# Kernel optimization log

Hardware: AMD Instinct MI355X
Metric: run time of the kernel (lower is better)

The kernel has to match this reference:

```python
import jax, jax.numpy as jnp
import numpy as np

N_NODES = 4096
N_EDGES = 16384
L = 512
MP_STEPS = 5
DT = 0.01


def _mlp(x, W1, b1, W2, b2):
    return jax.nn.relu(x @ W1 + b1) @ W2 + b2


def _ln(x):
    m = jnp.mean(x, axis=-1, keepdims=True)
    v = jnp.var(x, axis=-1, keepdims=True)
    return (x - m) * jax.lax.rsqrt(v + 1e-6)


_PARAM_SHAPES = [
    ("enc_e_W1", (1, L)), ("enc_e_b1", (L,)), ("enc_e_W2", (L, L)), ("enc_e_b2", (L,)),
    ("enc_n_W1", (1, L)), ("enc_n_b1", (L,)), ("enc_n_W2", (L, L)), ("enc_n_b2", (L,)),
    ("proc_e_W1", (3 * L, L)), ("proc_e_b1", (L,)), ("proc_e_W2", (L, L)), ("proc_e_b2", (L,)),
    ("proc_n_W1", (2 * L, L)), ("proc_n_b1", (L,)), ("proc_n_W2", (L, L)), ("proc_n_b2", (L,)),
    ("dec_e_W1", (L, L)), ("dec_e_b1", (L,)), ("dec_e_W2", (L, 1)), ("dec_e_b2", (1,)),
]


def setup_inputs() -> dict:
    key = jax.random.key(0)
    ks = jax.random.split(key, 3 + len(_PARAM_SHAPES))
    d = {}
    d["state"] = jax.random.normal(ks[0], (N_EDGES + N_NODES,), dtype=jnp.float32)
    d["senders"] = jax.random.randint(ks[1], (N_EDGES,), 0, N_NODES)
    d["receivers"] = jax.random.randint(ks[2], (N_EDGES,), 0, N_NODES)
    for i, (name, shp) in enumerate(_PARAM_SHAPES):
        if name.endswith(("b1", "b2")):
            d[name] = jnp.zeros(shp, dtype=jnp.float32)
        else:
            d[name] = 0.02 * jax.random.normal(ks[3 + i], shp, dtype=jnp.float32)
    return d


def _hamiltonian(x, senders, receivers,
                 enc_e_W1, enc_e_b1, enc_e_W2, enc_e_b2,
                 enc_n_W1, enc_n_b1, enc_n_W2, enc_n_b2,
                 proc_e_W1, proc_e_b1, proc_e_W2, proc_e_b2,
                 proc_n_W1, proc_n_b1, proc_n_W2, proc_n_b2,
                 dec_e_W1, dec_e_b1, dec_e_W2, dec_e_b2):
    # graph_from_state: edge scalars then node scalars
    e = x[:N_EDGES].reshape(N_EDGES, 1)
    n = x[N_EDGES:].reshape(N_NODES, 1)
    # encode (MLP + layer norm)
    eh = _ln(_mlp(e, enc_e_W1, enc_e_b1, enc_e_W2, enc_e_b2))  # [E, L]
    nh = _ln(_mlp(n, enc_n_W1, enc_n_b1, enc_n_W2, enc_n_b2))  # [N, L]
    # process: num_mp_steps of GraphNetwork-style message passing, shared params
    for _ in range(MP_STEPS):
        msg_in = jnp.concatenate([eh, nh[senders], nh[receivers]], axis=-1)  # [E, 3L]
        eh = eh + _mlp(msg_in, proc_e_W1, proc_e_b1, proc_e_W2, proc_e_b2)
        agg = jax.ops.segment_sum(eh, receivers, num_segments=N_NODES)  # [N, L]
        node_in = jnp.concatenate([nh, agg], axis=-1)  # [N, 2L]
        nh = nh + _mlp(node_in, proc_n_W1, proc_n_b1, proc_n_W2, proc_n_b2)
    # decode edges to scalars; H = sum of decoded edge energies
    dec_e = _mlp(eh, dec_e_W1, dec_e_b1, dec_e_W2, dec_e_b2)  # [E, 1]
    return jnp.sum(dec_e)


def reference(state, senders, receivers,
              enc_e_W1, enc_e_b1, enc_e_W2, enc_e_b2,
              enc_n_W1, enc_n_b1, enc_n_W2, enc_n_b2,
              proc_e_W1, proc_e_b1, proc_e_W2, proc_e_b2,
              proc_n_W1, proc_n_b1, proc_n_W2, proc_n_b2,
              dec_e_W1, dec_e_b1, dec_e_W2, dec_e_b2):
    def H_fn(x):
        return _hamiltonian(x, senders, receivers,
                            enc_e_W1, enc_e_b1, enc_e_W2, enc_e_b2,
                            enc_n_W1, enc_n_b1, enc_n_W2, enc_n_b2,
                            proc_e_W1, proc_e_b1, proc_e_W2, proc_e_b2,
                            proc_n_W1, proc_n_b1, proc_n_W2, proc_n_b2,
                            dec_e_W1, dec_e_b1, dec_e_W2, dec_e_b2)
    H, dH = jax.value_and_grad(H_fn)(state)
    # one integrator step driven by the Hamiltonian gradient (stand-in for DAE solve)
    next_state = state - DT * dH
    return next_state
```

## Files before the change

### kernel.cpp

```cpp
#include <hip/hip_runtime.h>


#define E_ROWS 16384
#define N_ROWS 4096
#define ALL_ROWS 20480
#define DT_F   0.01f

typedef unsigned char u8;
typedef unsigned short u16;
typedef unsigned long long u64;
typedef __attribute__((ext_vector_type(8))) short short8v;
typedef __attribute__((ext_vector_type(4))) float f32x4;

__device__ __forceinline__ u16 f2b(float f) {
    union { float f; unsigned u; } v; v.f = f;
    unsigned r = v.u + 0x7FFF + ((v.u >> 16) & 1);
    return (u16)(r >> 16);
}
__device__ __forceinline__ float b2f(u16 u) {
    union { unsigned u; float f; } v; v.u = ((unsigned)u) << 16;
    return v.f;
}
__device__ __forceinline__ void gld16(const u16* g, u16* l) {
    __builtin_amdgcn_global_load_lds((const __attribute__((address_space(1))) void*)g,
                                     (__attribute__((address_space(3))) void*)l, 16, 0, 0);
}
template<int N> __device__ __forceinline__ void waitcnt_vm() {
    if constexpr (N == 0)      asm volatile("s_waitcnt vmcnt(0)" ::: "memory");
    else if constexpr (N == 2) asm volatile("s_waitcnt vmcnt(2)" ::: "memory");
    else if constexpr (N == 4) asm volatile("s_waitcnt vmcnt(4)" ::: "memory");
    else if constexpr (N == 8) asm volatile("s_waitcnt vmcnt(8)" ::: "memory");
}

template<int BM, int WM, int WN, int KTOT, int LDA, int LDC,
         bool ADD_C, bool GATHER2, bool BIAS, bool RELU_MASK, bool APPLY_MASK,
         bool WF32, bool WBF16, bool DUALOUT, bool ROWDOT, bool DECW2, bool BSEL>
__global__ __launch_bounds__(256)
void bgemm(const u16* __restrict__ A, const u16* __restrict__ Bt, const u16* __restrict__ Bt2,
           float* __restrict__ C, u16* __restrict__ Cb,
           const u16* __restrict__ Cinb, const float* __restrict__ bias,
           const float* __restrict__ bias2, const u16* __restrict__ G12b,
           const int* __restrict__ sidx, const int* __restrict__ ridx,
           u8* __restrict__ maskw, u16* __restrict__ C2b,
           const float* __restrict__ wvec, const float* __restrict__ wvec2,
           float* __restrict__ outp)
{
    constexpr int BN = WN * 64;
    constexpr int NA = BM / 16;
    constexpr int TC = (BM + BN) / 16;
    constexpr int PER = TC / 4;
    constexpr int NT = KTOT / 32;
    constexpr int IFRAG = BM / WM / 16;
    constexpr int BUFU = TC * 512;
    constexpr int LSZ = (3 * BUFU > BM * BN) ? 3 * BUFU : BM * BN;
    __shared__ u16 Ls[LSZ];

    const int tid = threadIdx.x;
    const int lane = tid & 63;
    const int wv = tid >> 6;
    const int wr = wv / WN;
    const int wc = wv % WN;

    const int gx = gridDim.x;
    int id = blockIdx.y * gx + blockIdx.x;
    const int nwg = gx * gridDim.y;
    id = (id & 7) * (nwg >> 3) + (id >> 3);
    const int bx = id % gx;
    const int by = id / gx;
    const int rowBase = by * BM;
    const int colBase = bx * BN;

    const u16* BtU = Bt;
    const float* biasU = bias;
    const float* wvecU = wvec;
    if (BSEL && rowBase >= E_ROWS) { BtU = Bt2; biasU = bias2; wvecU = wvec2; }

    const int srow = lane & 15;
    const int slotk = (lane >> 4) << 3;

    const u16* srcs[PER];
    int dstoff[PER];
#pragma unroll
    for (int q = 0; q < PER; ++q) {
        const int c = wv + (q << 2);
        if (c < NA)
            srcs[q] = A + (size_t)(rowBase + c * 16 + srow) * LDA + slotk;
        else
            srcs[q] = BtU + (size_t)(colBase + (c - NA) * 16 + srow) * KTOT + slotk;
        dstoff[q] = c * 512;
    }

    f32x4 acc[IFRAG][4];
#pragma unroll
    for (int i = 0; i < IFRAG; ++i)
#pragma unroll
        for (int j = 0; j < 4; ++j)
            acc[i][j] = (f32x4){0.f, 0.f, 0.f, 0.f};

    const int fro = ((lane >> 4) << 7) + ((lane & 15) << 3);

#pragma unroll
    for (int q = 0; q < PER; ++q) gld16(srcs[q], &Ls[dstoff[q]]);
#pragma unroll
    for (int q = 0; q < PER; ++q) gld16(srcs[q] + 32, &Ls[BUFU + dstoff[q]]);
    waitcnt_vm<PER>();
    __builtin_amdgcn_s_barrier();
    asm volatile("" ::: "memory");

    for (int t = 0; t < NT; ++t) {
        const int cur = t % 3;
        if (t + 2 < NT) {
            const int nxt = (t + 2) % 3;
#pragma unroll
            for (int q = 0; q < PER; ++q)
                gld16(srcs[q] + (t + 2) * 32, &Ls[nxt * BUFU + dstoff[q]]);
        }
        const u16* Lc = &Ls[cur * BUFU];
        short8v af[IFRAG], bfm[4];
#pragma unroll
        for (int i = 0; i < IFRAG; ++i)
            af[i] = *(const short8v*)&Lc[((wr * IFRAG + i) << 9) + fro];
#pragma unroll
        for (int j = 0; j < 4; ++j)
            bfm[j] = *(const short8v*)&Lc[((NA + (wc << 2) + j) << 9) + fro];
#pragma unroll
        for (int i = 0; i < IFRAG; ++i)
#pragma unroll
            for (int j = 0; j < 4; ++j)
                acc[i][j] = __builtin_amdgcn_mfma_f32_16x16x32_bf16(af[i], bfm[j], acc[i][j], 0, 0, 0);
        if (t + 1 < NT) {
            if (t + 2 < NT) waitcnt_vm<PER>();
            else            waitcnt_vm<0>();
            __builtin_amdgcn_s_barrier();
            asm volatile("" ::: "memory");
        }
    }
    __syncthreads();

    if constexpr (WF32) {
        const int colB = colBase + wc * 64 + (lane & 15);
        const int rowB = rowBase + wr * (BM / WM) + ((lane >> 4) << 2);
        float bcol[4];
#pragma unroll
        for (int j = 0; j < 4; ++j) bcol[j] = biasU[colB + (j << 4)];
#pragma unroll
        for (int i = 0; i < IFRAG; ++i)
#pragma unroll
            for (int r = 0; r < 4; ++r) {
                const int row = rowB + (i << 4) + r;
#pragma unroll
                for (int j = 0; j < 4; ++j)
                    C[(size_t)row * LDC + colB + (j << 4)] = acc[i][j][r] + bcol[j];
            }
    } else {
        const int colL = wc * 64 + (lane & 15);
        const int rowL0 = wr * (BM / WM) + ((lane >> 4) << 2);
#pragma unroll
        for (int i = 0; i < IFRAG; ++i)
#pragma unroll
            for (int r = 0; r < 4; ++r) {
                const int row = rowL0 + (i << 4) + r;
#pragma unroll
                for (int j = 0; j < 4; ++j) {
                    const int col = colL + (j << 4);
                    int byte = row * (BN * 2) + col * 2;
                    byte ^= (row & 7) << 4;
                    *(u16*)((char*)Ls + byte) = f2b(acc[i][j][r]);
                }
            }
        __syncthreads();

        constexpr int TPR = BN / 8;
        constexpr int RPP = 256 / TPR;
        constexpr int NP = BM / RPP;
        const int rloc = tid / TPR;
        const int seg = tid % TPR;
        const int col0 = seg * 8;
        const bool upper = DUALOUT && (colBase >= 512);
#pragma unroll
        for (int p = 0; p < NP; ++p) {
            const int row = p * RPP + rloc;
            const int grow = rowBase + row;
            const int gcol = colBase + col0;
            int byte = row * (BN * 2) + col0 * 2;
            byte ^= (row & 7) << 4;
            const short8v sv = *(const short8v*)((const char*)Ls + byte);
            float v[8];
#pragma unroll
            for (int e = 0; e < 8; ++e) v[e] = b2f((u16)sv[e]);

            if (DUALOUT && upper) {
                short8v res;
#pragma unroll
                for (int e = 0; e < 8; ++e) res[e] = (short)f2b(v[e]);
                *(short8v*)&C2b[(size_t)grow * 512 + (gcol - 512)] = res;
                continue;
            }
            if (GATHER2) {
                const int si = sidx[grow], ri = ridx[grow];
                const short8v g1 = *(const short8v*)&G12b[(size_t)si * 1024 + gcol];
                const short8v g2 = *(const short8v*)&G12b[(size_t)ri * 1024 + 512 + gcol];
#pragma unroll
                for (int e = 0; e < 8; ++e) v[e] += b2f((u16)g1[e]) + b2f((u16)g2[e]);
            }
            if (ADD_C) {
                const short8v c8 = *(const short8v*)&Cinb[(size_t)grow * LDC + gcol];
#pragma unroll
                for (int e = 0; e < 8; ++e) v[e] += b2f((u16)c8[e]);
            }
            if (BIAS) {
                const float4 b0 = *(const float4*)&biasU[gcol];
                const float4 b1 = *(const float4*)&biasU[gcol + 4];
                v[0] += b0.x; v[1] += b0.y; v[2] += b0.z; v[3] += b0.w;
                v[4] += b1.x; v[5] += b1.y; v[6] += b1.z; v[7] += b1.w;
            }
            if (DECW2) {
                const float4 w0 = *(const float4*)&wvecU[gcol];
                const float4 w1 = *(const float4*)&wvecU[gcol + 4];
                const float wl[8] = {w0.x, w0.y, w0.z, w0.w, w1.x, w1.y, w1.z, w1.w};
                short8v res;
#pragma unroll
                for (int e = 0; e < 8; ++e) res[e] = (v[e] > 0.f) ? (short)f2b(wl[e]) : (short)0;
                *(short8v*)&Cb[(size_t)grow * LDC + gcol] = res;
                continue;
            }
            if (RELU_MASK) {
                u64 mm = 0;
#pragma unroll
                for (int e = 0; e < 8; ++e) {
                    const bool m = v[e] > 0.f;
                    mm |= (u64)(m ? 1 : 0) << (e * 8);
                    if (!m) v[e] = 0.f;
                }
                *(u64*)&maskw[(size_t)grow * 512 + gcol] = mm;
            }
            if (APPLY_MASK) {
                const u64 mm = *(const u64*)&maskw[(size_t)grow * 512 + gcol];
#pragma unroll
                for (int e = 0; e < 8; ++e)
                    if (!((mm >> (e * 8)) & 0xff)) v[e] = 0.f;
            }
            if (ROWDOT) {
                const float4 w0 = *(const float4*)&wvecU[gcol];
                const float4 w1 = *(const float4*)&wvecU[gcol + 4];
                float rds = v[0] * w0.x + v[1] * w0.y + v[2] * w0.z + v[3] * w0.w
                          + v[4] * w1.x + v[5] * w1.y + v[6] * w1.z + v[7] * w1.w;
#pragma unroll
                for (int m = 1; m < TPR; m <<= 1) rds += __shfl_xor(rds, m);
                if (seg == 0) atomicAdd(outp + grow, -DT_F * rds);
            }
            if (WBF16) {
                short8v res;
#pragma unroll
                for (int e = 0; e < 8; ++e) res[e] = (short)f2b(v[e]);
                *(short8v*)&Cb[(size_t)grow * LDC + gcol] = res;
            }
        }
    }
}

struct WArgs {
    const float* src[10];
    u16* dstP[10];
    u16* dstT[10];
    int ldP[10], ldT[10];
};

__global__ void wcvt_kernel(WArgs a)
{
    const int i = blockIdx.z;
    const float* W = a.src[i];
    u16* P = a.dstP[i]; const int lp = a.ldP[i];
    u16* T = a.dstT[i]; const int lt = a.ldT[i];
    __shared__ u16 t[64][66];
    const int rb = blockIdx.y << 6, cb = blockIdx.x << 6;
    const int tr = threadIdx.x >> 4;
    const int tc = (threadIdx.x & 15) << 2;
#pragma unroll
    for (int rr = 0; rr < 4; ++rr) {
        const int r = tr + (rr << 4);
        const float4 v = *(const float4*)&W[(size_t)(rb + r) * 512 + cb + tc];
        ushort4 u; u.x = f2b(v.x); u.y = f2b(v.y); u.z = f2b(v.z); u.w = f2b(v.w);
        *(ushort4*)&P[(size_t)(rb + r) * lp + cb + tc] = u;
        t[r][tc] = u.x; t[r][tc + 1] = u.y; t[r][tc + 2] = u.z; t[r][tc + 3] = u.w;
    }
    __syncthreads();
#pragma unroll
    for (int rr = 0; rr < 4; ++rr) {
        const int n = tr + (rr << 4);
        ushort4 u;
        u.x = t[tc][n]; u.y = t[tc + 1][n]; u.z = t[tc + 2][n]; u.w = t[tc + 3][n];
        *(ushort4*)&T[(size_t)(cb + n) * lt + rb + tc] = u;
    }
}

__device__ void csr_build(const int* __restrict__ idx, int* __restrict__ starts,
                          int* __restrict__ eids)
{
    __shared__ int hist[4096];
    __shared__ int scanbuf[1024];
    const int t = threadIdx.x;
    for (int i = t; i < 4096; i += 1024) hist[i] = 0;
    __syncthreads();
    for (int e = t; e < 16384; e += 1024) atomicAdd(&hist[idx[e]], 1);
    __syncthreads();
    const int base = t << 2;
    const int l0 = hist[base], l1 = hist[base + 1], l2 = hist[base + 2], l3 = hist[base + 3];
    const int lsum = l0 + l1 + l2 + l3;
    scanbuf[t] = lsum;
    __syncthreads();
    for (int ofs = 1; ofs < 1024; ofs <<= 1) {
        const int v = scanbuf[t];
        const int u = (t >= ofs) ? scanbuf[t - ofs] : 0;
        __syncthreads();
        scanbuf[t] = v + u;
        __syncthreads();
    }
    const int excl = scanbuf[t] - lsum;
    const int p0 = excl, p1 = p0 + l0, p2 = p1 + l1, p3 = p2 + l2;
    starts[base] = p0; starts[base + 1] = p1; starts[base + 2] = p2; starts[base + 3] = p3;
    if (t == 0) starts[4096] = 16384;
    __syncthreads();
    hist[base] = p0; hist[base + 1] = p1; hist[base + 2] = p2; hist[base + 3] = p3;
    __syncthreads();
    for (int e = t; e < 16384; e += 1024) {
        const int pos = atomicAdd(&hist[idx[e]], 1);
        eids[pos] = e;
    }
    __syncthreads();
    for (int n = t; n < 4096; n += 1024) {
        const int s0 = starts[n], s1 = hist[n];
        for (int i = s0 + 1; i < s1; ++i) {
            const int v = eids[i];
            int j = i - 1;
            while (j >= s0 && eids[j] > v) { eids[j + 1] = eids[j]; --j; }
            eids[j + 1] = v;
        }
    }
}

__global__ __launch_bounds__(1024) void csr2_kernel(const int* __restrict__ senders,
                                                    const int* __restrict__ receivers,
                                                    int* __restrict__ sst, int* __restrict__ seid,
                                                    int* __restrict__ rst, int* __restrict__ reid)
{
    if (blockIdx.x == 0) csr_build(receivers, rst, reid);
    else                 csr_build(senders, sst, seid);
}

__global__ void init_out_kernel(const float* __restrict__ state, float* __restrict__ out)
{
    const int t = blockIdx.x * 256 + threadIdx.x;
    out[t] = state[t];
}

__global__ void seg_agg_fwd_kernel(const u16* __restrict__ ehb, const int* __restrict__ starts,
                                   const int* __restrict__ eids, const u16* __restrict__ nhb,
                                   u16* __restrict__ nagg)
{
    const int n = blockIdx.x, c = threadIdx.x;
    const int s0 = starts[n], s1 = starts[n + 1];
    float a0 = 0.f, a1 = 0.f;
    for (int i = s0; i < s1; ++i) {
        const u16* p = ehb + (size_t)eids[i] * 512;
        a0 += b2f(p[c]); a1 += b2f(p[c + 256]);
    }
    u16* d = nagg + (size_t)n * 1024;
    const u16* s = nhb + (size_t)n * 512;
    d[c] = s[c]; d[c + 256] = s[c + 256];
    d[512 + c] = f2b(a0); d[768 + c] = f2b(a1);
}

__global__ void seg_sr_bwd_kernel(const u16* __restrict__ dh1e,
                                  const int* __restrict__ sst, const int* __restrict__ seid,
                                  const int* __restrict__ rst, const int* __restrict__ reid,
                                  u16* __restrict__ SR)
{
    const int n = blockIdx.x, c = threadIdx.x;
    float a0 = 0.f, a1 = 0.f, b0 = 0.f, b1 = 0.f;
    for (int i = sst[n]; i < sst[n + 1]; ++i) {
        const u16* p = dh1e + (size_t)seid[i] * 512;
        a0 += b2f(p[c]); a1 += b2f(p[c + 256]);
    }
    for (int i = rst[n]; i < rst[n + 1]; ++i) {
        const u16* p = dh1e + (size_t)reid[i] * 512;
        b0 += b2f(p[c]); b1 += b2f(p[c + 256]);
    }
    u16* d = SR + (size_t)n * 1024;
    d[c] = f2b(a0); d[c + 256] = f2b(a1);
    d[512 + c] = f2b(b0); d[768 + c] = f2b(b1);
}

__global__ void enc_h1_kernel(const float* __restrict__ x,
                              const float* __restrict__ W1e, const float* __restrict__ b1e,
                              const float* __restrict__ W1n, const float* __restrict__ b1n,
                              u16* __restrict__ h1b, u8* __restrict__ mask)
{
    const int idx = blockIdx.x * 256 + threadIdx.x;
    const int row = idx >> 7;
    const int c = (idx & 127) << 2;
    const bool edge = row < E_ROWS;
    const float* W1 = edge ? W1e : W1n;
    const float* b1 = edge ? b1e : b1n;
    const float xv = x[row];
    const float4 w = *(const float4*)&W1[c];
    const float4 b = *(const float4*)&b1[c];
    float4 v;
    v.x = fmaf(xv, w.x, b.x); v.y = fmaf(xv, w.y, b.y);
    v.z = fmaf(xv, w.z, b.z); v.w = fmaf(xv, w.w, b.w);
    uchar4 m;
    m.x = v.x > 0.f; m.y = v.y > 0.f; m.z = v.z > 0.f; m.w = v.w > 0.f;
    v.x = m.x ? v.x : 0.f; v.y = m.y ? v.y : 0.f;
    v.z = m.z ? v.z : 0.f; v.w = m.w ? v.w : 0.f;
    const size_t o = (size_t)row * 512 + c;
    ushort4 u; u.x = f2b(v.x); u.y = f2b(v.y); u.z = f2b(v.z); u.w = f2b(v.w);
    *(ushort4*)&h1b[o] = u;
    *(uchar4*)&mask[o] = m;
}

__global__ void ln_fwd_kernel(const float* __restrict__ x, u16* __restrict__ xhat_b,
                              u16* __restrict__ xb, float* __restrict__ rstd_save)
{
    const int row = blockIdx.x, tid = threadIdx.x;
    const float* p = x + (size_t)row * 512;
    const float a = p[tid], b = p[tid + 256];
    __shared__ float s1[256], s2[256];
    s1[tid] = a + b; s2[tid] = a * a + b * b;
    __syncthreads();
    for (int d = 128; d > 0; d >>= 1) {
        if (tid < d) { s1[tid] += s1[tid + d]; s2[tid] += s2[tid + d]; }
        __syncthreads();
    }
    const float mean = s1[0] * (1.f / 512.f);
    const float var = s2[0] * (1.f / 512.f) - mean * mean;
    const float r = rsqrtf(var + 1e-6f);
    const float ya = (a - mean) * r, yb = (b - mean) * r;
    const size_t o = (size_t)row * 512 + tid;
    xhat_b[o] = f2b(ya); xhat_b[o + 256] = f2b(yb);
    xb[o] = f2b(ya); xb[o + 256] = f2b(yb);
    if (tid == 0) rstd_save[row] = r;
}

__global__ void ln_bwd_kernel(u16* __restrict__ d, const u16* __restrict__ xhat_b,
                              const float* __restrict__ rstd)
{
    const int row = blockIdx.x, tid = threadIdx.x;
    u16* p = d + (size_t)row * 512;
    const u16* xh = xhat_b + (size_t)row * 512;
    const float da = b2f(p[tid]), dbv = b2f(p[tid + 256]);
    const float xa = b2f(xh[tid]), xbv = b2f(xh[tid + 256]);
    __shared__ float s1[256], s2[256];
    s1[tid] = da + dbv; s2[tid] = da * xa + dbv * xbv;
    __syncthreads();
    for (int dd = 128; dd > 0; dd >>= 1) {
        if (tid < dd) { s1[tid] += s1[tid + dd]; s2[tid] += s2[tid + dd]; }
        __syncthreads();
    }
    const float m1 = s1[0] * (1.f / 512.f);
    const float m2 = s2[0] * (1.f / 512.f);
    const float r = rstd[row];
    p[tid] = f2b(r * (da - m1 - xa * m2));
    p[tid + 256] = f2b(r * (dbv - m1 - xbv * m2));
}

__global__ void gather_add_kernel(u16* __restrict__ dst, const u16* __restrict__ src,
                                  const int* __restrict__ idx)
{
    const int t = blockIdx.x * 256 + threadIdx.x;
    const int row = t >> 6;
    const int c = (t & 63) << 3;
    const size_t o = (size_t)row * 512 + c;
    short8v a = *(const short8v*)&dst[o];
    const short8v g = *(const short8v*)&src[(size_t)idx[row] * 512 + c];
    short8v r;
#pragma unroll
    for (int i = 0; i < 8; ++i)
        r[i] = (short)f2b(b2f((u16)a[i]) + b2f((u16)g[i]));
    *(short8v*)&dst[o] = r;
}

extern "C" void kernel_launch(void* const* d_in, const int* in_sizes, int n_in,
                              void* d_out, int out_size, void* d_ws, size_t ws_size,
                              hipStream_t stream)
{
    (void)in_sizes; (void)n_in; (void)out_size; (void)ws_size;
    const float* state     = (const float*)d_in[0];
    const int*   senders   = (const int*)d_in[1];
    const int*   receivers = (const int*)d_in[2];
    const float* enc_e_W1 = (const float*)d_in[3];
    const float* enc_e_b1 = (const float*)d_in[4];
    const float* enc_e_W2 = (const float*)d_in[5];
    const float* enc_e_b2 = (const float*)d_in[6];
    const float* enc_n_W1 = (const float*)d_in[7];
    const float* enc_n_b1 = (const float*)d_in[8];
    const float* enc_n_W2 = (const float*)d_in[9];
    const float* enc_n_b2 = (const float*)d_in[10];
    const float* pe_W1 = (const float*)d_in[11];
    const float* pe_b1 = (const float*)d_in[12];
    const float* pe_W2 = (const float*)d_in[13];
    const float* pe_b2 = (const float*)d_in[14];
    const float* pn_W1 = (const float*)d_in[15];
    const float* pn_b1 = (const float*)d_in[16];
    const float* pn_W2 = (const float*)d_in[17];
    const float* pn_b2 = (const float*)d_in[18];
    const float* de_W1 = (const float*)d_in[19];
    const float* de_b1 = (const float*)d_in[20];
    const float* de_W2 = (const float*)d_in[21];
    float* out = (float*)d_out;

    const size_t EL = (size_t)E_ROWS * 512, NL = (size_t)N_ROWS * 512;
    const size_t AL = (size_t)ALL_ROWS * 512;
    const size_t LL = 512 * 512;
    char* w = (char*)d_ws;
    size_t off = 0;
    auto carve = [&](size_t bytes) -> char* {
        char* p = w + off;
        off += (bytes + 255) & ~(size_t)255;
        return p;
    };
    u16* wb = (u16*)carve(20 * LL * 2);
    u16* WT0 = wb;           u16* WT1 = wb + LL;      u16* WT2 = wb + 2 * LL;
    u16* WT34 = wb + 3 * LL;                          u16* WT5 = wb + 5 * LL;
    u16* WT8 = wb + 6 * LL;  u16* WT9 = wb + 7 * LL;
    u16* WP0 = wb + 8 * LL;  u16* WP1 = wb + 9 * LL;  u16* WP2 = wb + 10 * LL;
    u16* WP5 = wb + 11 * LL; u16* WP8 = wb + 12 * LL; u16* WP9 = wb + 13 * LL;
    u16* WT67 = wb + 14 * LL;
    u16* WP34c = wb + 16 * LL;
    u16* WP67 = wb + 18 * LL;

    float* eh  = (float*)carve(AL * 4);
    u16* ehb   = (u16*)carve(EL * 2);
    u16* nhb   = (u16*)carve(NL * 2);
    u16* h1eb  = (u16*)carve(EL * 2);
    u16* h1nb  = (u16*)carve(NL * 2);
    u16* eh0b  = (u16*)carve(EL * 2);
    u16* nh0b  = (u16*)carve(NL * 2);
    u8* menc   = (u8*)carve(AL);
    u16* G1b   = (u16*)carve(NL * 2);
    u16* G12b  = (u16*)carve(NL * 2 * 2);
    u16* nsr   = (u16*)carve(NL * 2 * 2);
    float* rstd = (float*)carve(ALL_ROWS * 4);
    u8* mpe    = (u8*)carve(5 * EL);
    u8* mpn    = (u8*)carve(5 * NL);
    int* rst  = (int*)carve(4097 * 4);
    int* reid = (int*)carve(16384 * 4);
    int* sst  = (int*)carve(4097 * 4);
    int* seid = (int*)carve(16384 * 4);

    const dim3 blk(256);
    const dim3 gE(4, E_ROWS / 128);
    const dim3 gA(4, ALL_ROWS / 128);
    const dim3 gN512(8, N_ROWS / 64);
    const dim3 gN1024(16, N_ROWS / 64);
    const float* fp = nullptr;
    u16* up = nullptr;
    const u16* cup = nullptr;
    const int* ip = nullptr;
    u8* mp = nullptr;
    float* f2p = nullptr;

    WArgs wa;
    const float* wsrc[10] = { enc_e_W2, enc_n_W2, pe_W1, pe_W1 + LL, pe_W1 + 2 * LL,
                              pe_W2, pn_W1, pn_W1 + LL, pn_W2, de_W1 };
    u16* dstP[10] = { WP0, WP1, WP2, WP34c, WP34c + 512, WP5, WP67, WP67 + LL, WP8, WP9 };
    int  ldP [10] = { 512, 512, 512, 1024,  1024,        512, 512,  512,       512, 512 };
    u16* dstT[10] = { WT0, WT1, WT2, WT34, WT34 + LL, WT5, WT67, WT67 + 512, WT8, WT9 };
    int  ldT [10] = { 512, 512, 512, 512,  512,       512, 1024, 1024,       512, 512 };
    for (int i = 0; i < 10; ++i) {
        wa.src[i] = wsrc[i]; wa.dstP[i] = dstP[i]; wa.dstT[i] = dstT[i];
        wa.ldP[i] = ldP[i]; wa.ldT[i] = ldT[i];
    }
    wcvt_kernel<<<dim3(8, 8, 10), blk, 0, stream>>>(wa);

    csr2_kernel<<<2, 1024, 0, stream>>>(senders, receivers, sst, seid, rst, reid);
    init_out_kernel<<<ALL_ROWS / 256, blk, 0, stream>>>(state, out);

    enc_h1_kernel<<<ALL_ROWS * 128 / 256, blk, 0, stream>>>(state, enc_e_W1, enc_e_b1,
                                                            enc_n_W1, enc_n_b1, h1eb, menc);
    bgemm<128,2,2,512,512,512, false,false,true,false,false, true,false,false,false,false,true>
        <<<gA, blk, 0, stream>>>(h1eb, WT0, WT1, eh, up, cup, enc_e_b2, enc_n_b2, cup, ip, ip, mp, up, fp, fp, f2p);
    ln_fwd_kernel<<<ALL_ROWS, blk, 0, stream>>>(eh, eh0b, ehb, rstd);

    for (int k = 0; k < 5; ++k) {
        bgemm<64,4,1,512,512,1024, false,false,false,false,false, false,true,false,false,false,false>
            <<<gN1024, blk, 0, stream>>>(nhb, WT34, cup, f2p, G12b, cup, fp, fp, cup, ip, ip, mp, up, fp, fp, f2p);
        bgemm<128,2,2,512,512,512, false,true,true,true,false, false,true,false,false,false,false>
            <<<gE, blk, 0, stream>>>(ehb, WT2, cup, f2p, h1eb, cup, pe_b1, fp, G12b, senders, receivers, mpe + (size_t)k * EL, up, fp, fp, f2p);
        bgemm<128,2,2,512,512,512, true,false,true,false,false, false,true,false,false,false,false>
            <<<gE, blk, 0, stream>>>(h1eb, WT5, cup, f2p, ehb, ehb, pe_b2, fp, cup, ip, ip, mp, up, fp, fp, f2p);
        seg_agg_fwd_kernel<<<N_ROWS, blk, 0, stream>>>(ehb, rst, reid, nhb, nsr);
        bgemm<64,4,1,1024,1024,512, false,false,true,true,false, false,true,false,false,false,false>
            <<<gN512, blk, 0, stream>>>(nsr, WT67, cup, f2p, h1nb, cup, pn_b1, fp, cup, ip, ip, mpn + (size_t)k * NL, up, fp, fp, f2p);
        bgemm<64,4,1,512,512,512, true,false,true,false,false, false,true,false,false,false,false>
            <<<gN512, blk, 0, stream>>>(h1nb, WT8, cup, f2p, nhb, nhb, pn_b2, fp, cup, ip, ip, mp, up, fp, fp, f2p);
    }

    bgemm<128,2,2,512,512,512, false,false,true,false,false, false,false,false,false,true,false>
        <<<gE, blk, 0, stream>>>(ehb, WT9, cup, f2p, h1eb, cup, de_b1, fp, cup, ip, ip, mp, up, de_W2, fp, f2p);

    bgemm<128,2,2,512,512,512, false,false,false,false,false, false,true,false,false,false,false>
        <<<gE, blk, 0, stream>>>(h1eb, WP9, cup, f2p, ehb, cup, fp, fp, cup, ip, ip, mp, up, fp, fp, f2p);

    for (int k = 4; k >= 0; --k) {
        if (k < 4) {
            bgemm<64,4,1,512,512,512, false,false,false,false,true, false,true,false,false,false,false>
                <<<gN512, blk, 0, stream>>>(nhb, WP8, cup, f2p, h1nb, cup, fp, fp, cup, ip, ip, mpn + (size_t)k * NL, up, fp, fp, f2p);
            bgemm<64,4,1,512,512,512, true,false,false,false,false, false,true,true,false,false,false>
                <<<gN1024, blk, 0, stream>>>(h1nb, WP67, cup, f2p, nhb, nhb, fp, fp, cup, ip, ip, mp, G1b, fp, fp, f2p);
            gather_add_kernel<<<E_ROWS * 64 / 256, blk, 0, stream>>>(ehb, G1b, receivers);
        }
        bgemm<128,2,2,512,512,512, false,false,false,false,true, false,true,false,false,false,false>
            <<<gE, blk, 0, stream>>>(ehb, WP5, cup, f2p, h1eb, cup, fp, fp, cup, ip, ip, mpe + (size_t)k * EL, up, fp, fp, f2p);
        bgemm<128,2,2,512,512,512, true,false,false,false,false, false,true,false,false,false,false>
            <<<gE, blk, 0, stream>>>(h1eb, WP2, cup, f2p, ehb, ehb, fp, fp, cup, ip, ip, mp, up, fp, fp, f2p);
        seg_sr_bwd_kernel<<<N_ROWS, blk, 0, stream>>>(h1eb, sst, seid, rst, reid, nsr);
        if (k == 4)
            bgemm<64,4,1,1024,1024,512, false,false,false,false,false, false,true,false,false,false,false>
                <<<gN512, blk, 0, stream>>>(nsr, WP34c, cup, f2p, nhb, cup, fp, fp, cup, ip, ip, mp, up, fp, fp, f2p);
        else
            bgemm<64,4,1,1024,1024,512, true,false,false,false,false, false,true,false,false,false,false>
                <<<gN512, blk, 0, stream>>>(nsr, WP34c, cup, f2p, nhb, nhb, fp, fp, cup, ip, ip, mp, up, fp, fp, f2p);
    }

    ln_bwd_kernel<<<ALL_ROWS, blk, 0, stream>>>(ehb, eh0b, rstd);
    bgemm<128,2,2,512,512,512, false,false,false,false,true, false,false,false,true,false,true>
        <<<gA, blk, 0, stream>>>(ehb, WP0, WP1, f2p, up, cup, fp, fp, cup, ip, ip, menc, up, enc_e_W1, enc_n_W1, out);
}
```

Before: 1.237 ms.

## Bit-pack ReLU masks and merge backward node GEMM into edge GEMM launch

```diff
diff --git a/kernel.cpp b/kernel.cpp
--- a/kernel.cpp
+++ b/kernel.cpp
@@ -34,7 +34,8 @@
 
 template<int BM, int WM, int WN, int KTOT, int LDA, int LDC,
          bool ADD_C, bool GATHER2, bool BIAS, bool RELU_MASK, bool APPLY_MASK,
-         bool WF32, bool WBF16, bool DUALOUT, bool ROWDOT, bool DECW2, bool BSEL>
+         bool WF32, bool WBF16, bool DUALOUT, bool ROWDOT, bool DECW2, bool BSEL,
+         bool MERGE_SR>
 __global__ __launch_bounds__(256)
 void bgemm(const u16* __restrict__ A, const u16* __restrict__ Bt, const u16* __restrict__ Bt2,
            float* __restrict__ C, u16* __restrict__ Cb,
@@ -43,13 +44,14 @@
            const int* __restrict__ sidx, const int* __restrict__ ridx,
            u8* __restrict__ maskw, u16* __restrict__ C2b,
            const float* __restrict__ wvec, const float* __restrict__ wvec2,
-           float* __restrict__ outp)
+           float* __restrict__ outp,
+           const u16* __restrict__ A2, const u16* __restrict__ Cin2,
+           u16* __restrict__ Cb2)
 {
     constexpr int BN = WN * 64;
     constexpr int NA = BM / 16;
     constexpr int TC = (BM + BN) / 16;
     constexpr int PER = TC / 4;
-    constexpr int NT = KTOT / 32;
     constexpr int IFRAG = BM / WM / 16;
     constexpr int BUFU = TC * 512;
     constexpr int LSZ = (3 * BUFU > BM * BN) ? 3 * BUFU : BM * BN;
@@ -67,8 +69,10 @@
     id = (id & 7) * (nwg >> 3) + (id >> 3);
     const int bx = id % gx;
     const int by = id / gx;
-    const int rowBase = by * BM;
     const int colBase = bx * BN;
+
+    const bool isSR = MERGE_SR && (by < 32);
+    const int rowBase = MERGE_SR ? (isSR ? by * BM : (by - 32) * BM) : by * BM;
 
     const u16* BtU = Bt;
     const float* biasU = bias;
@@ -77,16 +81,24 @@
 
     const int srow = lane & 15;
     const int slotk = (lane >> 4) << 3;
+    const int nt = (MERGE_SR && isSR) ? 32 : (KTOT / 32);
 
     const u16* srcs[PER];
     int dstoff[PER];
 #pragma unroll
     for (int q = 0; q < PER; ++q) {
         const int c = wv + (q << 2);
-        if (c < NA)
-            srcs[q] = A + (size_t)(rowBase + c * 16 + srow) * LDA + slotk;
-        else
-            srcs[q] = BtU + (size_t)(colBase + (c - NA) * 16 + srow) * KTOT + slotk;
+        if (MERGE_SR && isSR) {
+            if (c < NA)
+                srcs[q] = A2 + (size_t)(rowBase + c * 16 + srow) * 1024 + slotk;
+            else
+                srcs[q] = Bt2 + (size_t)(colBase + (c - NA) * 16 + srow) * 1024 + slotk;
+        } else {
+            if (c < NA)
+                srcs[q] = A + (size_t)(rowBase + c * 16 + srow) * LDA + slotk;
+            else
+                srcs[q] = BtU + (size_t)(colBase + (c - NA) * 16 + srow) * KTOT + slotk;
+        }
         dstoff[q] = c * 512;
     }
 
@@ -107,9 +119,9 @@
     __builtin_amdgcn_s_barrier();
     asm volatile("" ::: "memory");
 
-    for (int t = 0; t < NT; ++t) {
+    for (int t = 0; t < nt; ++t) {
         const int cur = t % 3;
-        if (t + 2 < NT) {
+        if (t + 2 < nt) {
             const int nxt = (t + 2) % 3;
 #pragma unroll
             for (int q = 0; q < PER; ++q)
@@ -128,8 +140,8 @@
 #pragma unroll
             for (int j = 0; j < 4; ++j)
                 acc[i][j] = __builtin_amdgcn_mfma_f32_16x16x32_bf16(af[i], bfm[j], acc[i][j], 0, 0, 0);
-        if (t + 1 < NT) {
-            if (t + 2 < NT) waitcnt_vm<PER>();
+        if (t + 1 < nt) {
+            if (t + 2 < nt) waitcnt_vm<PER>();
             else            waitcnt_vm<0>();
             __builtin_amdgcn_s_barrier();
             asm volatile("" ::: "memory");
@@ -189,6 +201,18 @@
 #pragma unroll
             for (int e = 0; e < 8; ++e) v[e] = b2f((u16)sv[e]);
 
+            if (MERGE_SR && isSR) {
+                if (Cin2) {
+                    const short8v c8 = *(const short8v*)&Cin2[(size_t)grow * 512 + gcol];
+#pragma unroll
+                    for (int e = 0; e < 8; ++e) v[e] += b2f((u16)c8[e]);
+                }
+                short8v res;
+#pragma unroll
+                for (int e = 0; e < 8; ++e) res[e] = (short)f2b(v[e]);
+                *(short8v*)&Cb2[(size_t)grow * 512 + gcol] = res;
+                continue;
+            }
             if (DUALOUT && upper) {
                 short8v res;
 #pragma unroll
@@ -225,20 +249,20 @@
                 continue;
             }
             if (RELU_MASK) {
-                u64 mm = 0;
+                u8 mm = 0;
 #pragma unroll
                 for (int e = 0; e < 8; ++e) {
                     const bool m = v[e] > 0.f;
-                    mm |= (u64)(m ? 1 : 0) << (e * 8);
+                    mm |= (u8)(m ? 1 : 0) << e;
                     if (!m) v[e] = 0.f;
                 }
-                *(u64*)&maskw[(size_t)grow * 512 + gcol] = mm;
+                maskw[(size_t)grow * 64 + (gcol >> 3)] = mm;
             }
             if (APPLY_MASK) {
-                const u64 mm = *(const u64*)&maskw[(size_t)grow * 512 + gcol];
+                const u8 mm = maskw[(size_t)grow * 64 + (gcol >> 3)];
 #pragma unroll
                 for (int e = 0; e < 8; ++e)
-                    if (!((mm >> (e * 8)) & 0xff)) v[e] = 0.f;
+                    if (!((mm >> e) & 1)) v[e] = 0.f;
             }
             if (ROWDOT) {
                 const float4 w0 = *(const float4*)&wvecU[gcol];
@@ -397,25 +421,29 @@
                               u16* __restrict__ h1b, u8* __restrict__ mask)
 {
     const int idx = blockIdx.x * 256 + threadIdx.x;
-    const int row = idx >> 7;
-    const int c = (idx & 127) << 2;
+    const int row = idx >> 6;
+    const int c = (idx & 63) << 3;
     const bool edge = row < E_ROWS;
     const float* W1 = edge ? W1e : W1n;
     const float* b1 = edge ? b1e : b1n;
     const float xv = x[row];
-    const float4 w = *(const float4*)&W1[c];
-    const float4 b = *(const float4*)&b1[c];
-    float4 v;
-    v.x = fmaf(xv, w.x, b.x); v.y = fmaf(xv, w.y, b.y);
-    v.z = fmaf(xv, w.z, b.z); v.w = fmaf(xv, w.w, b.w);
-    uchar4 m;
-    m.x = v.x > 0.f; m.y = v.y > 0.f; m.z = v.z > 0.f; m.w = v.w > 0.f;
-    v.x = m.x ? v.x : 0.f; v.y = m.y ? v.y : 0.f;
-    v.z = m.z ? v.z : 0.f; v.w = m.w ? v.w : 0.f;
-    const size_t o = (size_t)row * 512 + c;
-    ushort4 u; u.x = f2b(v.x); u.y = f2b(v.y); u.z = f2b(v.z); u.w = f2b(v.w);
-    *(ushort4*)&h1b[o] = u;
-    *(uchar4*)&mask[o] = m;
+    const float4 w0 = *(const float4*)&W1[c];
+    const float4 w1 = *(const float4*)&W1[c + 4];
+    const float4 bb0 = *(const float4*)&b1[c];
+    const float4 bb1 = *(const float4*)&b1[c + 4];
+    const float wl[8] = {w0.x, w0.y, w0.z, w0.w, w1.x, w1.y, w1.z, w1.w};
+    const float bl[8] = {bb0.x, bb0.y, bb0.z, bb0.w, bb1.x, bb1.y, bb1.z, bb1.w};
+    short8v h;
+    u8 mm = 0;
+#pragma unroll
+    for (int e = 0; e < 8; ++e) {
+        float v = fmaf(xv, wl[e], bl[e]);
+        const bool m = v > 0.f;
+        mm |= (u8)(m ? 1 : 0) << e;
+        h[e] = m ? (short)f2b(v) : (short)0;
+    }
+    *(short8v*)&h1b[(size_t)row * 512 + c] = h;
+    mask[(size_t)row * 64 + (c >> 3)] = mm;
 }
 
 __global__ void ln_fwd_kernel(const float* __restrict__ x, u16* __restrict__ xhat_b,
@@ -535,20 +563,23 @@
     u16* h1nb  = (u16*)carve(NL * 2);
     u16* eh0b  = (u16*)carve(EL * 2);
     u16* nh0b  = (u16*)carve(NL * 2);
-    u8* menc   = (u8*)carve(AL);
+    u8* menc   = (u8*)carve(AL / 8);
     u16* G1b   = (u16*)carve(NL * 2);
     u16* G12b  = (u16*)carve(NL * 2 * 2);
     u16* nsr   = (u16*)carve(NL * 2 * 2);
     float* rstd = (float*)carve(ALL_ROWS * 4);
-    u8* mpe    = (u8*)carve(5 * EL);
-    u8* mpn    = (u8*)carve(5 * NL);
+    u8* mpe    = (u8*)carve(5 * EL / 8);
+    u8* mpn    = (u8*)carve(5 * NL / 8);
     int* rst  = (int*)carve(4097 * 4);
     int* reid = (int*)carve(16384 * 4);
     int* sst  = (int*)carve(4097 * 4);
     int* seid = (int*)carve(16384 * 4);
 
+    const size_t ELM = EL / 8, NLM = NL / 8;
+
     const dim3 blk(256);
     const dim3 gE(4, E_ROWS / 128);
+    const dim3 gM(4, 32 + E_ROWS / 128);
     const dim3 gA(4, ALL_ROWS / 128);
     const dim3 gN512(8, N_ROWS / 64);
     const dim3 gN1024(16, N_ROWS / 64);
@@ -575,54 +606,49 @@
     csr2_kernel<<<2, 1024, 0, stream>>>(senders, receivers, sst, seid, rst, reid);
     init_out_kernel<<<ALL_ROWS / 256, blk, 0, stream>>>(state, out);
 
-    enc_h1_kernel<<<ALL_ROWS * 128 / 256, blk, 0, stream>>>(state, enc_e_W1, enc_e_b1,
-                                                            enc_n_W1, enc_n_b1, h1eb, menc);
-    bgemm<128,2,2,512,512,512, false,false,true,false,false, true,false,false,false,false,true>
-        <<<gA, blk, 0, stream>>>(h1eb, WT0, WT1, eh, up, cup, enc_e_b2, enc_n_b2, cup, ip, ip, mp, up, fp, fp, f2p);
+    enc_h1_kernel<<<ALL_ROWS * 64 / 256, blk, 0, stream>>>(state, enc_e_W1, enc_e_b1,
+                                                           enc_n_W1, enc_n_b1, h1eb, menc);
+    bgemm<128,2,2,512,512,512, false,false,true,false,false, true,false,false,false,false,true,false>
+        <<<gA, blk, 0, stream>>>(h1eb, WT0, WT1, eh, up, cup, enc_e_b2, enc_n_b2, cup, ip, ip, mp, up, fp, fp, f2p, cup, cup, up);
     ln_fwd_kernel<<<ALL_ROWS, blk, 0, stream>>>(eh, eh0b, ehb, rstd);
 
     for (int k = 0; k < 5; ++k) {
-        bgemm<64,4,1,512,512,1024, false,false,false,false,false, false,true,false,false,false,false>
-            <<<gN1024, blk, 0, stream>>>(nhb, WT34, cup, f2p, G12b, cup, fp, fp, cup, ip, ip, mp, up, fp, fp, f2p);
-        bgemm<128,2,2,512,512,512, false,true,true,true,false, false,true,false,false,false,false>
-            <<<gE, blk, 0, stream>>>(ehb, WT2, cup, f2p, h1eb, cup, pe_b1, fp, G12b, senders, receivers, mpe + (size_t)k * EL, up, fp, fp, f2p);
-        bgemm<128,2,2,512,512,512, true,false,true,false,false, false,true,false,false,false,false>
-            <<<gE, blk, 0, stream>>>(h1eb, WT5, cup, f2p, ehb, ehb, pe_b2, fp, cup, ip, ip, mp, up, fp, fp, f2p);
+        bgemm<64,4,1,512,512,1024, false,false,false,false,false, false,true,false,false,false,false,false>
+            <<<gN1024, blk, 0, stream>>>(nhb, WT34, cup, f2p, G12b, cup, fp, fp, cup, ip, ip, mp, up, fp, fp, f2p, cup, cup, up);
+        bgemm<128,2,2,512,512,512, false,true,true,true,false, false,true,false,false,false,false,false>
+            <<<gE, blk, 0, stream>>>(ehb, WT2, cup, f2p, h1eb, cup, pe_b1, fp, G12b, senders, receivers, mpe + (size_t)k * ELM, up, fp, fp, f2p, cup, cup, up);
+        bgemm<128,2,2,512,512,512, true,false,true,false,false, false,true,false,false,false,false,false>
+            <<<gE, blk, 0, stream>>>(h1eb, WT5, cup, f2p, ehb, ehb, pe_b2, fp, cup, ip, ip, mp, up, fp, fp, f2p, cup, cup, up);
         seg_agg_fwd_kernel<<<N_ROWS, blk, 0, stream>>>(ehb, rst, reid, nhb, nsr);
-        bgemm<64,4,1,1024,1024,512, false,false,true,true,false, false,true,false,false,false,false>
-            <<<gN512, blk, 0, stream>>>(nsr, WT67, cup, f2p, h1nb, cup, pn_b1, fp, cup, ip, ip, mpn + (size_t)k * NL, up, fp, fp, f2p);
-        bgemm<64,4,1,512,512,512, true,false,true,false,false, false,true,false,false,false,false>
-            <<<gN512, blk, 0, stream>>>(h1nb, WT8, cup, f2p, nhb, nhb, pn_b2, fp, cup, ip, ip, mp, up, fp, fp, f2p);
-    }
-
-    bgemm<128,2,2,512,512,512, false,false,true,false,false, false,false,false,false,true,false>
-        <<<gE, blk, 0, stream>>>(ehb, WT9, cup, f2p, h1eb, cup, de_b1, fp, cup, ip, ip, mp, up, de_W2, fp, f2p);
-
-    bgemm<128,2,2,512,512,512, false,false,false,false,false, false,true,false,false,false,false>
-        <<<gE, blk, 0, stream>>>(h1eb, WP9, cup, f2p, ehb, cup, fp, fp, cup, ip, ip, mp, up, fp, fp, f2p);
+        bgemm<64,4,1,1024,1024,512, false,false,true,true,false, false,true,false,false,false,false,false>
+            <<<gN512, blk, 0, stream>>>(nsr, WT67, cup, f2p, h1nb, cup, pn_b1, fp, cup, ip, ip, mpn + (size_t)k * NLM, up, fp, fp, f2p, cup, cup, up);
+        bgemm<64,4,1,512,512,512, true,false,true,false,false, false,true,false,false,false,false,false>
+            <<<gN512, blk, 0, stream>>>(h1nb, WT8, cup, f2p, nhb, nhb, pn_b2, fp, cup, ip, ip, mp, up, fp, fp, f2p, cup, cup, up);
+    }
+
+    bgemm<128,2,2,512,512,512, false,false,true,false,false, false,false,false,false,true,false,false>
+        <<<gE, blk, 0, stream>>>(ehb, WT9, cup, f2p, h1eb, cup, de_b1, fp, cup, ip, ip, mp, up, de_W2, fp, f2p, cup, cup, up);
+
+    bgemm<128,2,2,512,512,512, false,false,false,false,false, false,true,false,false,false,false,false>
+        <<<gE, blk, 0, stream>>>(h1eb, WP9, cup, f2p, ehb, cup, fp, fp, cup, ip, ip, mp, up, fp, fp, f2p, cup, cup, up);
 
     for (int k = 4; k >= 0; --k) {
         if (k < 4) {
-            bgemm<64,4,1,512,512,512, false,false,false,false,true, false,true,false,false,false,false>
-                <<<gN512, blk, 0, stream>>>(nhb, WP8, cup, f2p, h1nb, cup, fp, fp, cup, ip, ip, mpn + (size_t)k * NL, up, fp, fp, f2p);
-            bgemm<64,4,1,512,512,512, true,false,false,false,false, false,true,true,false,false,false>
-                <<<gN1024, blk, 0, stream>>>(h1nb, WP67, cup, f2p, nhb, nhb, fp, fp, cup, ip, ip, mp, G1b, fp, fp, f2p);
+            bgemm<64,4,1,512,512,512, false,false,false,false,true, false,true,false,false,false,false,false>
+                <<<gN512, blk, 0, stream>>>(nhb, WP8, cup, f2p, h1nb, cup, fp, fp, cup, ip, ip, mpn + (size_t)k * NLM, up, fp, fp, f2p, cup, cup, up);
+            bgemm<64,4,1,512,512,512, true,false,false,false,false, false,true,true,false,false,false,false>
+                <<<gN1024, blk, 0, stream>>>(h1nb, WP67, cup, f2p, nhb, nhb, fp, fp, cup, ip, ip, mp, G1b, fp, fp, f2p, cup, cup, up);
             gather_add_kernel<<<E_ROWS * 64 / 256, blk, 0, stream>>>(ehb, G1b, receivers);
         }
-        bgemm<128,2,2,512,512,512, false,false,false,false,true, false,true,false,false,false,false>
-            <<<gE, blk, 0, stream>>>(ehb, WP5, cup, f2p, h1eb, cup, fp, fp, cup, ip, ip, mpe + (size_t)k * EL, up, fp, fp, f2p);
-        bgemm<128,2,2,512,512,512, true,false,false,false,false, false,true,false,false,false,false>
-            <<<gE, blk, 0, stream>>>(h1eb, WP2, cup, f2p, ehb, ehb, fp, fp, cup, ip, ip, mp, up, fp, fp, f2p);
+        bgemm<128,2,2,512,512,512, false,false,false,false,true, false,true,false,false,false,false,false>
+            <<<gE, blk, 0, stream>>>(ehb, WP5, cup, f2p, h1eb, cup, fp, fp, cup, ip, ip, mpe + (size_t)k * ELM, up, fp, fp, f2p, cup, cup, up);
         seg_sr_bwd_kernel<<<N_ROWS, blk, 0, stream>>>(h1eb, sst, seid, rst, reid, nsr);
-        if (k == 4)
-            bgemm<64,4,1,1024,1024,512, false,false,false,false,false, false,true,false,false,false,false>
-                <<<gN512, blk, 0, stream>>>(nsr, WP34c, cup, f2p, nhb, cup, fp, fp, cup, ip, ip, mp, up, fp, fp, f2p);
-        else
-            bgemm<64,4,1,1024,1024,512, true,false,false,false,false, false,true,false,false,false,false>
-                <<<gN512, blk, 0, stream>>>(nsr, WP34c, cup, f2p, nhb, nhb, fp, fp, cup, ip, ip, mp, up, fp, fp, f2p);
+        bgemm<128,2,2,512,512,512, true,false,false,false,false, false,true,false,false,false,false,true>
+            <<<gM, blk, 0, stream>>>(h1eb, WP2, WP34c, f2p, ehb, ehb, fp, fp, cup, ip, ip, mp, up, fp, fp, f2p,
+                                     nsr, (k == 4) ? cup : nhb, nhb);
     }
 
     ln_bwd_kernel<<<ALL_ROWS, blk, 0, stream>>>(ehb, eh0b, rstd);
-    bgemm<128,2,2,512,512,512, false,false,false,false,true, false,false,false,true,false,true>
-        <<<gA, blk, 0, stream>>>(ehb, WP0, WP1, f2p, up, cup, fp, fp, cup, ip, ip, menc, up, enc_e_W1, enc_n_W1, out);
-}
+    bgemm<128,2,2,512,512,512, false,false,false,false,true, false,false,false,true,false,true,false>
+        <<<gA, blk, 0, stream>>>(ehb, WP0, WP1, f2p, up, cup, fp, fp, cup, ip, ip, menc, up, enc_e_W1, enc_n_W1, out, cup, cup, up);
+}
```

After: 1.286 ms. 1.04x slower.
